# Optimization experiments

Hardware: AMD Instinct MI355X
Metric: run time of the kernel (lower is better)

Reference implementation:

```python
import jax, jax.numpy as jnp
import numpy as np

# --- constants matching DILConfig ---
N_DIFF = 1000      # num_diffusion_steps
STEPS = 4          # inference_steps
S_MAX = 4          # max_scales
BUDGET = 0.2       # entropy_budget
G0 = 2.0           # guidance_strength
ENT_LO = 0.1       # stability_threshold_low
ENT_HI = 0.5       # stability_threshold_high
B, L, C, H = 16, 1024, 128, 512


def setup_inputs() -> dict:
    key = jax.random.key(0)
    ks = jax.random.split(key, 6)
    y_obs = jax.random.normal(ks[0], (B, L, C), dtype=jnp.float32)
    mask = (jax.random.uniform(ks[1], (B, L, C)) > 0.5).astype(jnp.float32)
    z_init = jax.random.normal(ks[2], (B, L, C), dtype=jnp.float32)
    W1 = jax.random.normal(ks[3], (C, H), dtype=jnp.float32) / np.sqrt(C)
    b1 = jnp.zeros((H,), dtype=jnp.float32)
    W2 = jax.random.normal(ks[4], (H, C), dtype=jnp.float32) / np.sqrt(H)
    b2 = jnp.zeros((C,), dtype=jnp.float32)
    tw = jax.random.normal(ks[5], (H,), dtype=jnp.float32)
    return {"y_obs": y_obs, "mask": mask, "z_init": z_init,
            "W1": W1, "b1": b1, "W2": W2, "b2": b2, "tw": tw}


def _dil_forward(y_obs, mask, z_init, W1, b1, W2, b2, tw):
    # diffusion schedule (linear betas)
    betas = jnp.linspace(1e-4, 0.02, N_DIFF, dtype=jnp.float32)
    ac = jnp.cumprod(1.0 - betas)
    alpha = jnp.sqrt(ac)                     # sqrt_alphas_cumprod
    sigma = jnp.sqrt(1.0 - ac)               # sqrt_one_minus_alphas_cumprod
    lam = jnp.log(alpha) - jnp.log(sigma)    # log-SNR/2

    step = N_DIFF // STEPS
    ks = [N_DIFF - 1 - i * step for i in range(STEPS)]

    def score(z, k):
        # epsilon predictor: channel MLP with scalar time feature
        t_feat = jnp.float32(k) / N_DIFF
        h = jax.nn.gelu(jnp.einsum('blc,ch->blh', z, W1) + b1 + t_feat * tw)
        return jnp.einsum('blh,hc->blc', h, W2) + b2

    z = z_init
    for k in ks:  # fixed small unrolled loop over inference steps
        kp = max(k - step, 0)
        eps = score(z, k)                                   # [B,L,C]
        h_lam = lam[kp] - lam[k]
        base_a = alpha[kp] / alpha[k]
        base_b = sigma[kp] * (jnp.exp(h_lam) - 1.0)

        # entropy map: batch-mean |eps| per pixel
        ent_pix = jnp.mean(jnp.abs(eps), axis=0)            # [L,C]

        # self-guidance on observed entries
        obs_err = (z - y_obs) * mask
        guidance = -obs_err / (jnp.var(obs_err) + 1e-8)     # [B,L,C]

        z_new = z
        # coarse -> fine so finer-scale selected nodes overwrite coarser ones
        for s in range(S_MAX - 1, -1, -1):
            w = 2 ** s
            pooled = ent_pix.reshape(L // w, w, C // w, w).mean(axis=(1, 3))
            Knodes = max(1, int(BUDGET * pooled.size))
            _, idx = jax.lax.top_k(pooled.ravel(), Knodes)
            selg = jnp.zeros((pooled.size,), jnp.float32).at[idx].set(1.0)
            selg = selg.reshape(pooled.shape)
            sel = jnp.repeat(jnp.repeat(selg, w, axis=0), w, axis=1)     # [L,C]
            ent_up = jnp.repeat(jnp.repeat(pooled, w, axis=0), w, axis=1)

            # adaptive solver order from entropy stability thresholds
            order = (1.0 + (ent_up > ENT_LO).astype(jnp.float32)
                         + (ent_up > ENT_HI).astype(jnp.float32))
            corr = (1.0 + (order - 1.0) * 0.5 * h_lam
                        + (order - 1.0) * (order - 2.0) / 6.0 * h_lam ** 2)
            gs = G0 * ent_up / (ent_up + 1.0)               # adaptive guidance

            cand = base_a * z - base_b * (corr * eps) + gs * guidance
            z_new = jnp.where(sel[None, :, :] > 0, cand, z_new)
        z = z_new
    return z


def reference(y_obs, mask, z_init, W1, b1, W2, b2, tw):
    return _dil_forward(y_obs, mask, z_init, W1, b1, W2, b2, tw)
```

## Files before the change

### kernel.cpp

```cpp
#include <hip/hip_runtime.h>
#include <math.h>
#include <stdint.h>

#define L_DIM 1024
#define C_DIM 128
#define H_DIM 512
#define B_DIM 16
#define LC (L_DIM * C_DIM)
#define BLC (B_DIM * LC)

typedef __attribute__((ext_vector_type(8))) short short8;
typedef __attribute__((ext_vector_type(4))) float floatx4;

__device__ __forceinline__ unsigned fordbits(unsigned u) {
    return (u & 0x80000000u) ? ~u : (u | 0x80000000u);
}

__device__ __forceinline__ void split3(float x, unsigned& uh, unsigned& um,
                                       unsigned& ul) {
    uh = __float_as_uint(x);
    const float r1 = x - __uint_as_float(uh & 0xffff0000u);
    um = __float_as_uint(r1);
    const float r2 = r1 - __uint_as_float(um & 0xffff0000u);
    ul = __float_as_uint(r2);
}

__device__ __forceinline__ float gelu_fast(float x) {
    const float g = 0.7978845608028654f * (x + 0.044715f * x * x * x);
    const float e = __expf(2.0f * g);
    const float t = 1.0f - 2.0f / (e + 1.0f);
    return 0.5f * x * (1.0f + t);
}

__global__ __launch_bounds__(256) void wsplit_kernel(
    const float* __restrict__ W1, const float* __restrict__ W2,
    unsigned short* __restrict__ W1h, unsigned short* __restrict__ W1m,
    unsigned short* __restrict__ W1l, unsigned short* __restrict__ W2h,
    unsigned short* __restrict__ W2m, unsigned short* __restrict__ W2l) {
    const int t = blockIdx.x * 256 + threadIdx.x;
    unsigned uh, um, ul;
    if (t < 65536) {
        const int j = t & 7, lane = (t >> 3) & 63, nt = (t >> 9) & 31,
                  kt = (t >> 14) & 3;
        const int k = kt * 32 + (lane >> 4) * 8 + j;
        const int n = nt * 16 + (lane & 15);
        split3(W1[k * 512 + n], uh, um, ul);
        W1h[t] = (unsigned short)(uh >> 16);
        W1m[t] = (unsigned short)(um >> 16);
        W1l[t] = (unsigned short)(ul >> 16);
    } else {
        const int t2 = t - 65536;
        const int j = t2 & 7, lane = (t2 >> 3) & 63, nt = (t2 >> 9) & 7,
                  kt = (t2 >> 12) & 15;
        const int k = kt * 32 + (lane >> 4) * 8 + j;
        const int n = nt * 16 + (lane & 15);
        split3(W2[k * 128 + n], uh, um, ul);
        W2h[t2] = (unsigned short)(uh >> 16);
        W2m[t2] = (unsigned short)(um >> 16);
        W2l[t2] = (unsigned short)(ul >> 16);
    }
}

#define MFMA6(AH, AM, AL, BH, BM, BL, ACC)                                    \
    ACC = __builtin_amdgcn_mfma_f32_16x16x32_bf16(AL, BH, ACC, 0, 0, 0);      \
    ACC = __builtin_amdgcn_mfma_f32_16x16x32_bf16(AM, BM, ACC, 0, 0, 0);      \
    ACC = __builtin_amdgcn_mfma_f32_16x16x32_bf16(AH, BL, ACC, 0, 0, 0);      \
    ACC = __builtin_amdgcn_mfma_f32_16x16x32_bf16(AM, BH, ACC, 0, 0, 0);      \
    ACC = __builtin_amdgcn_mfma_f32_16x16x32_bf16(AH, BM, ACC, 0, 0, 0);      \
    ACC = __builtin_amdgcn_mfma_f32_16x16x32_bf16(AH, BH, ACC, 0, 0, 0);

__device__ __forceinline__ int swz(int row, int col) {
    return row * 128 + ((((col >> 3) ^ (row & 15))) << 3) + (col & 7);
}

template <int UPD>
__global__ __launch_bounds__(512, 4) void mlp_kernel(
    float* __restrict__ z, const float* __restrict__ y,
    const float* __restrict__ mk,
    const unsigned short* __restrict__ W1h, const unsigned short* __restrict__ W1m,
    const unsigned short* __restrict__ W1l, const unsigned short* __restrict__ W2h,
    const unsigned short* __restrict__ W2m, const unsigned short* __restrict__ W2l,
    const float* __restrict__ b1, const float* __restrict__ tw,
    const float* __restrict__ b2, float t_feat,
    float* __restrict__ eps_buf, float* __restrict__ ent,
    const float* __restrict__ cA, const float* __restrict__ cB,
    const float* __restrict__ cG, float* __restrict__ accum) {
    __shared__ unsigned short zA[3][4096];
    __shared__ unsigned short hA[3][4096];
    __shared__ float red1[8], red2[8];
    const int tid = threadIdx.x;
    const int w = tid >> 6, lane = tid & 63;
    const int quad = lane >> 4, m16 = lane & 15;
    const int l0 = blockIdx.x * 2;

    float s1 = 0.f, s2 = 0.f;
#pragma unroll
    for (int e = 0; e < 2; ++e) {
        const int f = tid * 8 + e * 4;
        const int r_ = f >> 7, cb = f & 127;
        const int b = r_ & 15, il = r_ >> 4, l = l0 + il;
        const size_t g = ((size_t)b * 1024 + l) * 128 + cb;
        float4 zv = *(const float4*)(z + g);
        const float4 yv = *(const float4*)(y + g);
        const float4 mv = *(const float4*)(mk + g);
        if (UPD) {
            const float4 ev = *(const float4*)(eps_buf + g);
            const int pix = l * 128 + cb;
            const float4 a4 = *(const float4*)(cA + pix);
            const float4 b4 = *(const float4*)(cB + pix);
            const float4 g4 = *(const float4*)(cG + pix);
            zv.x = a4.x * zv.x - b4.x * ev.x - g4.x * ((zv.x - yv.x) * mv.x);
            zv.y = a4.y * zv.y - b4.y * ev.y - g4.y * ((zv.y - yv.y) * mv.y);
            zv.z = a4.z * zv.z - b4.z * ev.z - g4.z * ((zv.z - yv.z) * mv.z);
            zv.w = a4.w * zv.w - b4.w * ev.w - g4.w * ((zv.w - yv.w) * mv.w);
            *(float4*)(z + g) = zv;
        }
        float oe;
        oe = (zv.x - yv.x) * mv.x; s1 += oe; s2 += oe * oe;
        oe = (zv.y - yv.y) * mv.y; s1 += oe; s2 += oe * oe;
        oe = (zv.z - yv.z) * mv.z; s1 += oe; s2 += oe * oe;
        oe = (zv.w - yv.w) * mv.w; s1 += oe; s2 += oe * oe;

        const int base = swz(r_, cb);
        const float xs[4] = {zv.x, zv.y, zv.z, zv.w};
        ushort4 vh, vm, vl;
        unsigned uh, um, ul;
        split3(xs[0], uh, um, ul); vh.x = uh >> 16; vm.x = um >> 16; vl.x = ul >> 16;
        split3(xs[1], uh, um, ul); vh.y = uh >> 16; vm.y = um >> 16; vl.y = ul >> 16;
        split3(xs[2], uh, um, ul); vh.z = uh >> 16; vm.z = um >> 16; vl.z = ul >> 16;
        split3(xs[3], uh, um, ul); vh.w = uh >> 16; vm.w = um >> 16; vl.w = ul >> 16;
        *(ushort4*)(&zA[0][base]) = vh;
        *(ushort4*)(&zA[1][base]) = vm;
        *(ushort4*)(&zA[2][base]) = vl;
    }
#pragma unroll
    for (int off = 32; off; off >>= 1) {
        s1 += __shfl_down(s1, off);
        s2 += __shfl_down(s2, off);
    }
    if (lane == 0) { red1[w] = s1; red2[w] = s2; }
    __syncthreads();
    if (tid == 0) {
        float a1 = 0.f, a2 = 0.f;
#pragma unroll
        for (int i = 0; i < 8; ++i) { a1 += red1[i]; a2 += red2[i]; }
        atomicAdd(&accum[0], a1);
        atomicAdd(&accum[1], a2);
    }

    floatx4 acc1[8];
#pragma unroll
    for (int i = 0; i < 8; ++i) acc1[i] = (floatx4){0.f, 0.f, 0.f, 0.f};

#pragma unroll
    for (int kt = 0; kt < 4; ++kt) {
        short8 Ah[2], Am[2], Al[2];
#pragma unroll
        for (int il = 0; il < 2; ++il) {
            const int fb = swz(il * 16 + m16, kt * 32 + quad * 8);
            Ah[il] = *(const short8*)(&zA[0][fb]);
            Am[il] = *(const short8*)(&zA[1][fb]);
            Al[il] = *(const short8*)(&zA[2][fb]);
        }
#pragma unroll
        for (int q = 0; q < 4; ++q) {
            const size_t off = ((size_t)(kt * 32 + q * 8 + w) * 64 + lane) * 8;
            const short8 bh = *(const short8*)(W1h + off);
            const short8 bm = *(const short8*)(W1m + off);
            const short8 bl = *(const short8*)(W1l + off);
#pragma unroll
            for (int il = 0; il < 2; ++il) {
                floatx4 a = acc1[q * 2 + il];
                MFMA6(Ah[il], Am[il], Al[il], bh, bm, bl, a);
                acc1[q * 2 + il] = a;
            }
        }
    }

    floatx4 acc2[2];
    acc2[0] = (floatx4){0.f, 0.f, 0.f, 0.f};
    acc2[1] = (floatx4){0.f, 0.f, 0.f, 0.f};

    for (int q = 0; q < 4; ++q) {
        __syncthreads();
        {
            const int colg = q * 128 + w * 16 + m16;
            const float bb = b1[colg] + t_feat * tw[colg];
            const int kcol = w * 16 + m16;
#pragma unroll
            for (int il = 0; il < 2; ++il) {
#pragma unroll
                for (int r = 0; r < 4; ++r) {
                    const float x = gelu_fast(acc1[q * 2 + il][r] + bb);
                    unsigned uh, um, ul;
                    split3(x, uh, um, ul);
                    const int idx = swz(il * 16 + quad * 4 + r, kcol);
                    hA[0][idx] = (unsigned short)(uh >> 16);
                    hA[1][idx] = (unsigned short)(um >> 16);
                    hA[2][idx] = (unsigned short)(ul >> 16);
                }
            }
        }
        __syncthreads();

#pragma unroll
        for (int ktl = 0; ktl < 4; ++ktl) {
            short8 Ah2[2], Am2[2], Al2[2];
#pragma unroll
            for (int il = 0; il < 2; ++il) {
                const int fb = swz(il * 16 + m16, ktl * 32 + quad * 8);
                Ah2[il] = *(const short8*)(&hA[0][fb]);
                Am2[il] = *(const short8*)(&hA[1][fb]);
                Al2[il] = *(const short8*)(&hA[2][fb]);
            }
            const size_t off =
                ((size_t)((q * 4 + ktl) * 8 + w) * 64 + lane) * 8;
            const short8 bh = *(const short8*)(W2h + off);
            const short8 bm = *(const short8*)(W2m + off);
            const short8 bl = *(const short8*)(W2l + off);
#pragma unroll
            for (int il = 0; il < 2; ++il) {
                floatx4 a = acc2[il];
                MFMA6(Ah2[il], Am2[il], Al2[il], bh, bm, bl, a);
                acc2[il] = a;
            }
        }
    }

    {
        const int col = w * 16 + m16;
        const float bb2 = b2[col];
#pragma unroll
        for (int il = 0; il < 2; ++il) {
            float pa = 0.f;
#pragma unroll
            for (int r = 0; r < 4; ++r) {
                const float e = acc2[il][r] + bb2;
                const int b = quad * 4 + r;
                eps_buf[((size_t)b * 1024 + l0 + il) * 128 + col] = e;
                pa += fabsf(e);
            }
            pa += __shfl_xor(pa, 16);
            pa += __shfl_xor(pa, 32);
            if (quad == 0) ent[(l0 + il) * 128 + col] = pa * (1.0f / 16.0f);
        }
    }
}


__global__ __launch_bounds__(256) void pools_kernel(
    const float* __restrict__ ent, float* __restrict__ p1,
    float* __restrict__ p2, float* __restrict__ p3,
    unsigned* __restrict__ ghist) {
    __shared__ unsigned lh[16384];
    const int tid = threadIdx.x;
    const int gid = blockIdx.x * 256 + tid;
    for (int i = tid; i < 16384; i += 256) lh[i] = 0u;
    __syncthreads();

    {
        const float2 ev = *(const float2*)(ent + (size_t)gid * 2);
        atomicAdd(&lh[fordbits(__float_as_uint(ev.x)) >> 18], 1u);
        atomicAdd(&lh[fordbits(__float_as_uint(ev.y)) >> 18], 1u);
    }
    if (gid < 32768) {
        const int r = gid >> 6, c = gid & 63;
        float s = 0.f;
#pragma unroll
        for (int ii = 0; ii < 2; ++ii)
#pragma unroll
            for (int jj = 0; jj < 2; ++jj)
                s += ent[((r * 2 + ii) << 7) + c * 2 + jj];
        p1[gid] = s * 0.25f;
    }
    if (gid < 8192) {
        const int r = gid >> 5, c = gid & 31;
        float s = 0.f;
#pragma unroll
        for (int ii = 0; ii < 4; ++ii)
#pragma unroll
            for (int jj = 0; jj < 4; ++jj)
                s += ent[((r * 4 + ii) << 7) + c * 4 + jj];
        p2[gid] = s * 0.0625f;
    }
    if (gid < 2048) {
        const int r = gid >> 4, c = gid & 15;
        float s = 0.f;
#pragma unroll
        for (int ii = 0; ii < 8; ++ii)
#pragma unroll
            for (int jj = 0; jj < 8; ++jj)
                s += ent[((r * 8 + ii) << 7) + c * 8 + jj];
        p3[gid] = s * (1.0f / 64.0f);
    }
    __syncthreads();
    for (int i = tid; i < 16384; i += 256) {
        const unsigned c = lh[i];
        if (c) atomicAdd(&ghist[i], c);
    }
}

#define CAND_CAP 16384

template <int NPT4, int N, unsigned K>
__device__ __forceinline__ void small_select(
    const float* __restrict__ data, unsigned* __restrict__ gout, const int t,
    const int w8, unsigned* __restrict__ histcand,
    unsigned* __restrict__ part, unsigned (*hrep)[512],
    unsigned* sh_b, unsigned* sh_krem, unsigned* sh_cnt, unsigned* sh_d,
    unsigned* sh_k2) {
    float4 xv[NPT4];
#pragma unroll
    for (int i = 0; i < NPT4; ++i) {
        const int idx4 = t + i * 1024;
        if (idx4 < (N >> 2)) xv[i] = ((const float4*)data)[idx4];
        else xv[i] = (float4){-1e30f, -1e30f, -1e30f, -1e30f};
    }
    unsigned u[NPT4 * 4];
#pragma unroll
    for (int i = 0; i < NPT4; ++i) {
        u[4 * i + 0] = fordbits(__float_as_uint(xv[i].x));
        u[4 * i + 1] = fordbits(__float_as_uint(xv[i].y));
        u[4 * i + 2] = fordbits(__float_as_uint(xv[i].z));
        u[4 * i + 3] = fordbits(__float_as_uint(xv[i].w));
    }
    if (t == 0) { *sh_b = 0u; *sh_krem = 1u; *sh_cnt = 0u; *sh_d = 0u; *sh_k2 = 1u; }
    for (int i = t; i < 16384; i += 1024) histcand[i] = 0u;
    __syncthreads();
#pragma unroll
    for (int j = 0; j < NPT4 * 4; ++j) atomicAdd(&histcand[u[j] >> 18], 1u);
    __syncthreads();
    {
        unsigned s = 0;
#pragma unroll
        for (int j = 0; j < 16; ++j) s += histcand[t * 16 + j];
        part[t] = s;
    }
    __syncthreads();
    for (int off = 1; off < 1024; off <<= 1) {
        const unsigned v = (t + off < 1024) ? part[t + off] : 0u;
        __syncthreads();
        part[t] += v;
        __syncthreads();
    }
    {
        const unsigned suf = part[t];
        const unsigned sufn = (t < 1023) ? part[t + 1] : 0u;
        if (suf >= K && sufn < K) {
            unsigned run = sufn;
            for (int b = 15; b >= 0; --b) {
                const unsigned hb = histcand[t * 16 + b];
                run += hb;
                if (run >= K) {
                    *sh_b = (unsigned)(t * 16 + b);
                    *sh_krem = K - (run - hb);
                    break;
                }
            }
        }
    }
    __syncthreads();
    const unsigned b14 = *sh_b;
    unsigned krem = *sh_krem;
    __syncthreads();
#pragma unroll
    for (int j = 0; j < NPT4 * 4; ++j)
        if ((u[j] >> 18) == b14) {
            const unsigned p = atomicAdd(sh_cnt, 1u);
            if (p < CAND_CAP) histcand[p] = u[j];
        }
    __syncthreads();
    const unsigned cnt = *sh_cnt;
    const bool inlds = (cnt <= CAND_CAP);
    for (int i = t; i < 4096; i += 1024) ((unsigned*)hrep)[i] = 0u;
    __syncthreads();
    if (inlds) {
        for (unsigned i = t; i < cnt; i += 1024)
            atomicAdd(&hrep[w8][(histcand[i] >> 9) & 511u], 1u);
    } else {
#pragma unroll
        for (int j = 0; j < NPT4 * 4; ++j)
            if ((u[j] >> 18) == b14)
                atomicAdd(&hrep[w8][(u[j] >> 9) & 511u], 1u);
    }
    __syncthreads();
    if (t < 512) {
        unsigned s = 0;
#pragma unroll
        for (int r = 0; r < 8; ++r) s += hrep[r][t];
        part[t] = s;
    }
    __syncthreads();
    for (int off = 1; off < 512; off <<= 1) {
        unsigned v = 0u;
        if (t < 512) v = (t + off < 512) ? part[t + off] : 0u;
        __syncthreads();
        if (t < 512) part[t] += v;
        __syncthreads();
    }
    if (t < 512) {
        const unsigned suf = part[t];
        const unsigned sufn = (t < 511) ? part[t + 1] : 0u;
        if (suf >= krem && sufn < krem) { *sh_d = (unsigned)t; *sh_k2 = krem - sufn; }
    }
    __syncthreads();
    const unsigned dA = *sh_d;
    krem = *sh_k2;
    __syncthreads();
    for (int i = t; i < 4096; i += 1024) ((unsigned*)hrep)[i] = 0u;
    __syncthreads();
    if (inlds) {
        for (unsigned i = t; i < cnt; i += 1024) {
            const unsigned c = histcand[i];
            if (((c >> 9) & 511u) == dA) atomicAdd(&hrep[w8][c & 511u], 1u);
        }
    } else {
#pragma unroll
        for (int j = 0; j < NPT4 * 4; ++j)
            if ((u[j] >> 18) == b14 && ((u[j] >> 9) & 511u) == dA)
                atomicAdd(&hrep[w8][u[j] & 511u], 1u);
    }
    __syncthreads();
    if (t < 512) {
        unsigned s = 0;
#pragma unroll
        for (int r = 0; r < 8; ++r) s += hrep[r][t];
        part[t] = s;
    }
    __syncthreads();
    for (int off = 1; off < 512; off <<= 1) {
        unsigned v = 0u;
        if (t < 512) v = (t + off < 512) ? part[t + off] : 0u;
        __syncthreads();
        if (t < 512) part[t] += v;
        __syncthreads();
    }
    if (t < 512) {
        const unsigned suf = part[t];
        const unsigned sufn = (t < 511) ? part[t + 1] : 0u;
        if (suf >= krem && sufn < krem)
            gout[0] = (b14 << 18) | (dA << 9) | (unsigned)t;
    }
}

__global__ __launch_bounds__(1024, 1) void thresh_kernel(
    const float* __restrict__ ent, const float* __restrict__ p1,
    const float* __restrict__ p2, const float* __restrict__ p3,
    const unsigned* __restrict__ ghist, unsigned* __restrict__ gprefix) {
    const int scale = blockIdx.x, t = threadIdx.x;
    __shared__ unsigned histcand[16384];
    __shared__ unsigned part[1024];
    __shared__ unsigned hrep[8][512];
    __shared__ unsigned sh_b, sh_krem, sh_cnt, sh_d, sh_k2;
    const int w8 = (t >> 6) & 7;

    if (scale == 1) {
        small_select<8, 32768, 6553u>(p1, &gprefix[1], t, w8, histcand, part,
                                      hrep, &sh_b, &sh_krem, &sh_cnt, &sh_d,
                                      &sh_k2);
        return;
    }
    if (scale == 2) {
        small_select<2, 8192, 1638u>(p2, &gprefix[2], t, w8, histcand, part,
                                     hrep, &sh_b, &sh_krem, &sh_cnt, &sh_d,
                                     &sh_k2);
        return;
    }
    if (scale == 3) {
        small_select<1, 2048, 409u>(p3, &gprefix[3], t, w8, histcand, part,
                                    hrep, &sh_b, &sh_krem, &sh_cnt, &sh_d,
                                    &sh_k2);
        return;
    }

    const unsigned K = 26214u;
    if (t == 0) { sh_b = 0u; sh_krem = 1u; sh_cnt = 0u; sh_d = 0u; sh_k2 = 1u; }

    {
        unsigned s = 0;
        const uint4* h4 = (const uint4*)(ghist + t * 16);
#pragma unroll
        for (int j = 0; j < 4; ++j) {
            const uint4 x = h4[j];
            s += x.x + x.y + x.z + x.w;
        }
        part[t] = s;
    }
    __syncthreads();
    for (int off = 1; off < 1024; off <<= 1) {
        const unsigned v = (t + off < 1024) ? part[t + off] : 0u;
        __syncthreads();
        part[t] += v;
        __syncthreads();
    }
    {
        const unsigned suf = part[t];
        const unsigned sufn = (t < 1023) ? part[t + 1] : 0u;
        if (suf >= K && sufn < K) {
            unsigned run = sufn;
            for (int b = 15; b >= 0; --b) {
                const unsigned hb = ghist[t * 16 + b];
                run += hb;
                if (run >= K) {
                    sh_b = (unsigned)(t * 16 + b);
                    sh_krem = K - (run - hb);
                    break;
                }
            }
        }
    }
    __syncthreads();
    const unsigned b14 = sh_b;
    unsigned krem = sh_krem;

    for (int base = 0; base < 32768; base += 8192) {
        float4 w4[8];
#pragma unroll
        for (int i = 0; i < 8; ++i)
            w4[i] = ((const float4*)ent)[base + i * 1024 + t];
#pragma unroll
        for (int i = 0; i < 8; ++i) {
            const float xs[4] = {w4[i].x, w4[i].y, w4[i].z, w4[i].w};
#pragma unroll
            for (int j = 0; j < 4; ++j) {
                const unsigned uu = fordbits(__float_as_uint(xs[j]));
                if ((uu >> 18) == b14) {
                    const unsigned p = atomicAdd(&sh_cnt, 1u);
                    if (p < CAND_CAP) histcand[p] = uu;
                }
            }
        }
    }
    __syncthreads();
    const unsigned cnt = sh_cnt;
    const bool inlds = (cnt <= CAND_CAP);

    for (int i = t; i < 4096; i += 1024) ((unsigned*)hrep)[i] = 0u;
    __syncthreads();
    if (inlds) {
        for (unsigned i = t; i < cnt; i += 1024)
            atomicAdd(&hrep[w8][(histcand[i] >> 9) & 511u], 1u);
    } else {
        for (int base = 0; base < 32768; base += 8192) {
            float4 w4[8];
#pragma unroll
            for (int i = 0; i < 8; ++i)
                w4[i] = ((const float4*)ent)[base + i * 1024 + t];
#pragma unroll
            for (int i = 0; i < 8; ++i) {
                const float xs[4] = {w4[i].x, w4[i].y, w4[i].z, w4[i].w};
#pragma unroll
                for (int j = 0; j < 4; ++j) {
                    const unsigned uu = fordbits(__float_as_uint(xs[j]));
                    if ((uu >> 18) == b14)
                        atomicAdd(&hrep[w8][(uu >> 9) & 511u], 1u);
                }
            }
        }
    }
    __syncthreads();
    if (t < 512) {
        unsigned s = 0;
#pragma unroll
        for (int r = 0; r < 8; ++r) s += hrep[r][t];
        part[t] = s;
    }
    __syncthreads();
    for (int off = 1; off < 512; off <<= 1) {
        unsigned v = 0u;
        if (t < 512) v = (t + off < 512) ? part[t + off] : 0u;
        __syncthreads();
        if (t < 512) part[t] += v;
        __syncthreads();
    }
    if (t < 512) {
        const unsigned suf = part[t];
        const unsigned sufn = (t < 511) ? part[t + 1] : 0u;
        if (suf >= krem && sufn < krem) { sh_d = (unsigned)t; sh_k2 = krem - sufn; }
    }
    __syncthreads();
    const unsigned dA = sh_d;
    krem = sh_k2;
    __syncthreads();

    for (int i = t; i < 4096; i += 1024) ((unsigned*)hrep)[i] = 0u;
    __syncthreads();
    if (inlds) {
        for (unsigned i = t; i < cnt; i += 1024) {
            const unsigned c = histcand[i];
            if (((c >> 9) & 511u) == dA) atomicAdd(&hrep[w8][c & 511u], 1u);
        }
    } else {
        for (int base = 0; base < 32768; base += 8192) {
            float4 w4[8];
#pragma unroll
            for (int i = 0; i < 8; ++i)
                w4[i] = ((const float4*)ent)[base + i * 1024 + t];
#pragma unroll
            for (int i = 0; i < 8; ++i) {
                const float xs[4] = {w4[i].x, w4[i].y, w4[i].z, w4[i].w};
#pragma unroll
                for (int j = 0; j < 4; ++j) {
                    const unsigned uu = fordbits(__float_as_uint(xs[j]));
                    if ((uu >> 18) == b14 && ((uu >> 9) & 511u) == dA)
                        atomicAdd(&hrep[w8][uu & 511u], 1u);
                }
            }
        }
    }
    __syncthreads();
    if (t < 512) {
        unsigned s = 0;
#pragma unroll
        for (int r = 0; r < 8; ++r) s += hrep[r][t];
        part[t] = s;
    }
    __syncthreads();
    for (int off = 1; off < 512; off <<= 1) {
        unsigned v = 0u;
        if (t < 512) v = (t + off < 512) ? part[t + off] : 0u;
        __syncthreads();
        if (t < 512) part[t] += v;
        __syncthreads();
    }
    if (t < 512) {
        const unsigned suf = part[t];
        const unsigned sufn = (t < 511) ? part[t + 1] : 0u;
        if (suf >= krem && sufn < krem)
            gprefix[0] = (b14 << 18) | (dA << 9) | (unsigned)t;
    }
}

__global__ __launch_bounds__(256) void coeff_kernel(
    const float* __restrict__ ent, const float* __restrict__ p1,
    const float* __restrict__ p2, const float* __restrict__ p3,
    const unsigned* __restrict__ gprefix, const float* __restrict__ accum_si,
    float* __restrict__ cA, float* __restrict__ cB, float* __restrict__ cG,
    unsigned* __restrict__ ghist, float base_a, float base_b, float h_lam) {
    const int i = blockIdx.x * 256 + threadIdx.x;
    if (i < 16384) ghist[i] = 0u;

    const unsigned t0 = gprefix[0], t1 = gprefix[1], t2 = gprefix[2],
                   t3 = gprefix[3];
    const float mean = accum_si[0] * (1.0f / (float)BLC);
    const float var = accum_si[1] * (1.0f / (float)BLC) - mean * mean;
    const float vinv = 1.0f / (var + 1e-8f);

    const int l = i >> 7, c = i & 127;
    float ent_v = 0.f;
    bool sel = false;
    const float v0 = ent[i];
    if (fordbits(__float_as_uint(v0)) >= t0) { ent_v = v0; sel = true; }
    else {
        const float v1 = p1[((l >> 1) << 6) + (c >> 1)];
        if (fordbits(__float_as_uint(v1)) >= t1) { ent_v = v1; sel = true; }
        else {
            const float v2 = p2[((l >> 2) << 5) + (c >> 2)];
            if (fordbits(__float_as_uint(v2)) >= t2) { ent_v = v2; sel = true; }
            else {
                const float v3 = p3[((l >> 3) << 4) + (c >> 3)];
                if (fordbits(__float_as_uint(v3)) >= t3) { ent_v = v3; sel = true; }
            }
        }
    }
    if (sel) {
        float corr;
        if (ent_v > 0.5f)
            corr = 1.0f + h_lam + h_lam * h_lam * (1.0f / 3.0f);
        else if (ent_v > 0.1f)
            corr = 1.0f + 0.5f * h_lam;
        else
            corr = 1.0f;
        cA[i] = base_a;
        cB[i] = base_b * corr;
        cG[i] = (2.0f * ent_v / (ent_v + 1.0f)) * vinv;
    } else {
        cA[i] = 1.0f;
        cB[i] = 0.f;
        cG[i] = 0.f;
    }
}

__global__ __launch_bounds__(256) void update_kernel(
    float* __restrict__ z, const float* __restrict__ y,
    const float* __restrict__ mk, const float* __restrict__ eps,
    const float* __restrict__ cA, const float* __restrict__ cB,
    const float* __restrict__ cG) {
    const int idx = blockIdx.x * 256 + threadIdx.x;
    const int p = idx & (LC - 1);
    const float zi = z[idx];
    z[idx] = cA[p] * zi - cB[p] * eps[idx] - cG[p] * ((zi - y[idx]) * mk[idx]);
}

extern "C" void kernel_launch(void* const* d_in, const int* in_sizes, int n_in,
                              void* d_out, int out_size, void* d_ws,
                              size_t ws_size, hipStream_t stream) {
    const float* y_obs = (const float*)d_in[0];
    const float* mask = (const float*)d_in[1];
    const float* z_init = (const float*)d_in[2];
    const float* W1 = (const float*)d_in[3];
    const float* b1 = (const float*)d_in[4];
    const float* W2 = (const float*)d_in[5];
    const float* b2 = (const float*)d_in[6];
    const float* tw = (const float*)d_in[7];
    float* z = (float*)d_out;
    float* ws = (float*)d_ws;

    float* eps = ws;
    float* ent = ws + 2097152;
    float* p1 = ws + 2228224;
    float* p2 = ws + 2260992;
    float* p3 = ws + 2269184;
    float* cA = ws + 2271232;
    float* cB = ws + 2402304;
    float* cG = ws + 2533376;
    float* accum = ws + 2664448;
    unsigned* gprefix = (unsigned*)(ws + 2664456);
    unsigned* ghist = (unsigned*)(ws + 2664460);
    unsigned short* W1h = (unsigned short*)(ws + 2680844);
    unsigned short* W1m = (unsigned short*)(ws + 2713612);
    unsigned short* W1l = (unsigned short*)(ws + 2746380);
    unsigned short* W2h = (unsigned short*)(ws + 2779148);
    unsigned short* W2m = (unsigned short*)(ws + 2811916);
    unsigned short* W2l = (unsigned short*)(ws + 2844684);

    float alpha_[1000], sigma_[1000], lam_[1000];
    {
        float ac = 1.0f;
        for (int i = 0; i < 1000; ++i) {
            const float beta = 1e-4f + (0.02f - 1e-4f) * ((float)i / 999.0f);
            ac = ac * (1.0f - beta);
            alpha_[i] = sqrtf(ac);
            sigma_[i] = sqrtf(1.0f - ac);
            lam_[i] = logf(alpha_[i]) - logf(sigma_[i]);
        }
    }
    float tf[4], hl[4], ba[4], bb[4];
    for (int si = 0; si < 4; ++si) {
        const int k = 999 - si * 250;
        const int kp = (k - 250 > 0) ? (k - 250) : 0;
        tf[si] = (float)k / 1000.0f;
        hl[si] = lam_[kp] - lam_[k];
        ba[si] = alpha_[kp] / alpha_[k];
        bb[si] = sigma_[kp] * (expf(hl[si]) - 1.0f);
    }

    hipMemcpyAsync(z, z_init, sizeof(float) * BLC, hipMemcpyDeviceToDevice,
                   stream);
    hipMemsetAsync(accum, 0, (8 + 4 + 16384) * sizeof(unsigned), stream);
    wsplit_kernel<<<512, 256, 0, stream>>>(W1, W2, W1h, W1m, W1l, W2h, W2m,
                                           W2l);

    for (int si = 0; si < 4; ++si) {
        if (si == 0) {
            mlp_kernel<0><<<512, 512, 0, stream>>>(
                z, y_obs, mask, W1h, W1m, W1l, W2h, W2m, W2l, b1, tw, b2,
                tf[0], eps, ent, cA, cB, cG, accum);
        } else {
            mlp_kernel<1><<<512, 512, 0, stream>>>(
                z, y_obs, mask, W1h, W1m, W1l, W2h, W2m, W2l, b1, tw, b2,
                tf[si], eps, ent, cA, cB, cG, accum + 2 * si);
        }
        pools_kernel<<<256, 256, 0, stream>>>(ent, p1, p2, p3, ghist);
        thresh_kernel<<<4, 1024, 0, stream>>>(ent, p1, p2, p3, ghist, gprefix);
        coeff_kernel<<<512, 256, 0, stream>>>(ent, p1, p2, p3, gprefix,
                                              accum + 2 * si, cA, cB, cG,
                                              ghist, ba[si], bb[si], hl[si]);
    }
    update_kernel<<<8192, 256, 0, stream>>>(z, y_obs, mask, eps, cA, cB, cG);
}
```

Baseline: 388.6 us.

## Remove memcpy/memset, fuse final update into coeff, double-buffer hidden LDS

The initial z copy and the accumulator memset are dropped: the first MLP steps read z_init directly and the weight-split kernel zeroes the accumulators. The final update kernel is folded into a templated coeff kernel that applies the per-pixel coefficients across the batch. The MLP's second GEMM now alternates between two LDS buffers for hidden activations, and one per-chunk __syncthreads is removed. The pooling histogram packs two 16-bit counts per shared word and uses vector loads. The lost barrier and the 16-bit counters carry race and overflow risk.

```diff
diff --git a/kernel.cpp b/kernel.cpp
--- a/kernel.cpp
+++ b/kernel.cpp
@@ -36,8 +36,10 @@
     const float* __restrict__ W1, const float* __restrict__ W2,
     unsigned short* __restrict__ W1h, unsigned short* __restrict__ W1m,
     unsigned short* __restrict__ W1l, unsigned short* __restrict__ W2h,
-    unsigned short* __restrict__ W2m, unsigned short* __restrict__ W2l) {
+    unsigned short* __restrict__ W2m, unsigned short* __restrict__ W2l,
+    unsigned* __restrict__ zeroblk) {
     const int t = blockIdx.x * 256 + threadIdx.x;
+    if (t < 16396) zeroblk[t] = 0u;
     unsigned uh, um, ul;
     if (t < 65536) {
         const int j = t & 7, lane = (t >> 3) & 63, nt = (t >> 9) & 31,
@@ -75,8 +77,8 @@
 
 template <int UPD>
 __global__ __launch_bounds__(512, 4) void mlp_kernel(
-    float* __restrict__ z, const float* __restrict__ y,
-    const float* __restrict__ mk,
+    float* __restrict__ z, const float* __restrict__ zr,
+    const float* __restrict__ y, const float* __restrict__ mk,
     const unsigned short* __restrict__ W1h, const unsigned short* __restrict__ W1m,
     const unsigned short* __restrict__ W1l, const unsigned short* __restrict__ W2h,
     const unsigned short* __restrict__ W2m, const unsigned short* __restrict__ W2l,
@@ -85,8 +87,7 @@
     float* __restrict__ eps_buf, float* __restrict__ ent,
     const float* __restrict__ cA, const float* __restrict__ cB,
     const float* __restrict__ cG, float* __restrict__ accum) {
-    __shared__ unsigned short zA[3][4096];
-    __shared__ unsigned short hA[3][4096];
+    __shared__ unsigned short lds2[2][3][4096];
     __shared__ float red1[8], red2[8];
     const int tid = threadIdx.x;
     const int w = tid >> 6, lane = tid & 63;
@@ -100,7 +101,7 @@
         const int r_ = f >> 7, cb = f & 127;
         const int b = r_ & 15, il = r_ >> 4, l = l0 + il;
         const size_t g = ((size_t)b * 1024 + l) * 128 + cb;
-        float4 zv = *(const float4*)(z + g);
+        float4 zv = *(const float4*)(zr + g);
         const float4 yv = *(const float4*)(y + g);
         const float4 mv = *(const float4*)(mk + g);
         if (UPD) {
@@ -129,9 +130,9 @@
         split3(xs[1], uh, um, ul); vh.y = uh >> 16; vm.y = um >> 16; vl.y = ul >> 16;
         split3(xs[2], uh, um, ul); vh.z = uh >> 16; vm.z = um >> 16; vl.z = ul >> 16;
         split3(xs[3], uh, um, ul); vh.w = uh >> 16; vm.w = um >> 16; vl.w = ul >> 16;
-        *(ushort4*)(&zA[0][base]) = vh;
-        *(ushort4*)(&zA[1][base]) = vm;
-        *(ushort4*)(&zA[2][base]) = vl;
+        *(ushort4*)(&lds2[0][0][base]) = vh;
+        *(ushort4*)(&lds2[0][1][base]) = vm;
+        *(ushort4*)(&lds2[0][2][base]) = vl;
     }
 #pragma unroll
     for (int off = 32; off; off >>= 1) {
@@ -158,9 +159,9 @@
 #pragma unroll
         for (int il = 0; il < 2; ++il) {
             const int fb = swz(il * 16 + m16, kt * 32 + quad * 8);
-            Ah[il] = *(const short8*)(&zA[0][fb]);
-            Am[il] = *(const short8*)(&zA[1][fb]);
-            Al[il] = *(const short8*)(&zA[2][fb]);
+            Ah[il] = *(const short8*)(&lds2[0][0][fb]);
+            Am[il] = *(const short8*)(&lds2[0][1][fb]);
+            Al[il] = *(const short8*)(&lds2[0][2][fb]);
         }
 #pragma unroll
         for (int q = 0; q < 4; ++q) {
@@ -181,8 +182,9 @@
     acc2[0] = (floatx4){0.f, 0.f, 0.f, 0.f};
     acc2[1] = (floatx4){0.f, 0.f, 0.f, 0.f};
 
+#pragma unroll
     for (int q = 0; q < 4; ++q) {
-        __syncthreads();
+        const int bi = (q & 1) ^ 1;
         {
             const int colg = q * 128 + w * 16 + m16;
             const float bb = b1[colg] + t_feat * tw[colg];
@@ -195,9 +197,9 @@
                     unsigned uh, um, ul;
                     split3(x, uh, um, ul);
                     const int idx = swz(il * 16 + quad * 4 + r, kcol);
-                    hA[0][idx] = (unsigned short)(uh >> 16);
-                    hA[1][idx] = (unsigned short)(um >> 16);
-                    hA[2][idx] = (unsigned short)(ul >> 16);
+                    lds2[bi][0][idx] = (unsigned short)(uh >> 16);
+                    lds2[bi][1][idx] = (unsigned short)(um >> 16);
+                    lds2[bi][2][idx] = (unsigned short)(ul >> 16);
                 }
             }
         }
@@ -209,9 +211,9 @@
 #pragma unroll
             for (int il = 0; il < 2; ++il) {
                 const int fb = swz(il * 16 + m16, ktl * 32 + quad * 8);
-                Ah2[il] = *(const short8*)(&hA[0][fb]);
-                Am2[il] = *(const short8*)(&hA[1][fb]);
-                Al2[il] = *(const short8*)(&hA[2][fb]);
+                Ah2[il] = *(const short8*)(&lds2[bi][0][fb]);
+                Am2[il] = *(const short8*)(&lds2[bi][1][fb]);
+                Al2[il] = *(const short8*)(&lds2[bi][2][fb]);
             }
             const size_t off =
                 ((size_t)((q * 4 + ktl) * 8 + w) * 64 + lane) * 8;
@@ -252,51 +254,56 @@
     const float* __restrict__ ent, float* __restrict__ p1,
     float* __restrict__ p2, float* __restrict__ p3,
     unsigned* __restrict__ ghist) {
-    __shared__ unsigned lh[16384];
+    __shared__ unsigned lh[8192];
     const int tid = threadIdx.x;
     const int gid = blockIdx.x * 256 + tid;
-    for (int i = tid; i < 16384; i += 256) lh[i] = 0u;
+    for (int i = tid; i < 8192; i += 256) lh[i] = 0u;
     __syncthreads();
 
     {
         const float2 ev = *(const float2*)(ent + (size_t)gid * 2);
-        atomicAdd(&lh[fordbits(__float_as_uint(ev.x)) >> 18], 1u);
-        atomicAdd(&lh[fordbits(__float_as_uint(ev.y)) >> 18], 1u);
+        const unsigned b0 = fordbits(__float_as_uint(ev.x)) >> 18;
+        const unsigned b1_ = fordbits(__float_as_uint(ev.y)) >> 18;
+        atomicAdd(&lh[b0 >> 1], 1u << ((b0 & 1) << 4));
+        atomicAdd(&lh[b1_ >> 1], 1u << ((b1_ & 1) << 4));
     }
     if (gid < 32768) {
         const int r = gid >> 6, c = gid & 63;
         float s = 0.f;
 #pragma unroll
-        for (int ii = 0; ii < 2; ++ii)
-#pragma unroll
-            for (int jj = 0; jj < 2; ++jj)
-                s += ent[((r * 2 + ii) << 7) + c * 2 + jj];
+        for (int ii = 0; ii < 2; ++ii) {
+            const float2 e = *(const float2*)(ent + (((r * 2 + ii) << 7) + c * 2));
+            s += e.x; s += e.y;
+        }
         p1[gid] = s * 0.25f;
     }
     if (gid < 8192) {
         const int r = gid >> 5, c = gid & 31;
         float s = 0.f;
 #pragma unroll
-        for (int ii = 0; ii < 4; ++ii)
-#pragma unroll
-            for (int jj = 0; jj < 4; ++jj)
-                s += ent[((r * 4 + ii) << 7) + c * 4 + jj];
+        for (int ii = 0; ii < 4; ++ii) {
+            const float4 e = *(const float4*)(ent + (((r * 4 + ii) << 7) + c * 4));
+            s += e.x; s += e.y; s += e.z; s += e.w;
+        }
         p2[gid] = s * 0.0625f;
     }
     if (gid < 2048) {
         const int r = gid >> 4, c = gid & 15;
         float s = 0.f;
 #pragma unroll
-        for (int ii = 0; ii < 8; ++ii)
-#pragma unroll
-            for (int jj = 0; jj < 8; ++jj)
-                s += ent[((r * 8 + ii) << 7) + c * 8 + jj];
+        for (int ii = 0; ii < 8; ++ii) {
+            const float4 ea = *(const float4*)(ent + (((r * 8 + ii) << 7) + c * 8));
+            const float4 eb = *(const float4*)(ent + (((r * 8 + ii) << 7) + c * 8 + 4));
+            s += ea.x; s += ea.y; s += ea.z; s += ea.w;
+            s += eb.x; s += eb.y; s += eb.z; s += eb.w;
+        }
         p3[gid] = s * (1.0f / 64.0f);
     }
     __syncthreads();
-    for (int i = tid; i < 16384; i += 256) {
-        const unsigned c = lh[i];
-        if (c) atomicAdd(&ghist[i], c);
+    for (int i = tid; i < 8192; i += 256) {
+        const unsigned v = lh[i];
+        if (v & 0xFFFFu) atomicAdd(&ghist[2 * i], v & 0xFFFFu);
+        if (v >> 16) atomicAdd(&ghist[2 * i + 1], v >> 16);
     }
 }
 
@@ -631,14 +638,17 @@
     }
 }
 
+template <int FINAL>
 __global__ __launch_bounds__(256) void coeff_kernel(
     const float* __restrict__ ent, const float* __restrict__ p1,
     const float* __restrict__ p2, const float* __restrict__ p3,
     const unsigned* __restrict__ gprefix, const float* __restrict__ accum_si,
     float* __restrict__ cA, float* __restrict__ cB, float* __restrict__ cG,
-    unsigned* __restrict__ ghist, float base_a, float base_b, float h_lam) {
+    unsigned* __restrict__ ghist, float* __restrict__ z,
+    const float* __restrict__ y, const float* __restrict__ mk,
+    const float* __restrict__ eps, float base_a, float base_b, float h_lam) {
     const int i = blockIdx.x * 256 + threadIdx.x;
-    if (i < 16384) ghist[i] = 0u;
+    if (!FINAL && i < 16384) ghist[i] = 0u;
 
     const unsigned t0 = gprefix[0], t1 = gprefix[1], t2 = gprefix[2],
                    t3 = gprefix[3];
@@ -663,6 +673,7 @@
             }
         }
     }
+    float ca, cb, cg;
     if (sel) {
         float corr;
         if (ent_v > 0.5f)
@@ -671,25 +682,22 @@
             corr = 1.0f + 0.5f * h_lam;
         else
             corr = 1.0f;
-        cA[i] = base_a;
-        cB[i] = base_b * corr;
-        cG[i] = (2.0f * ent_v / (ent_v + 1.0f)) * vinv;
+        ca = base_a;
+        cb = base_b * corr;
+        cg = (2.0f * ent_v / (ent_v + 1.0f)) * vinv;
     } else {
-        cA[i] = 1.0f;
-        cB[i] = 0.f;
-        cG[i] = 0.f;
-    }
-}
-
-__global__ __launch_bounds__(256) void update_kernel(
-    float* __restrict__ z, const float* __restrict__ y,
-    const float* __restrict__ mk, const float* __restrict__ eps,
-    const float* __restrict__ cA, const float* __restrict__ cB,
-    const float* __restrict__ cG) {
-    const int idx = blockIdx.x * 256 + threadIdx.x;
-    const int p = idx & (LC - 1);
-    const float zi = z[idx];
-    z[idx] = cA[p] * zi - cB[p] * eps[idx] - cG[p] * ((zi - y[idx]) * mk[idx]);
+        ca = 1.0f; cb = 0.f; cg = 0.f;
+    }
+    if (!FINAL) {
+        cA[i] = ca; cB[i] = cb; cG[i] = cg;
+    } else {
+#pragma unroll
+        for (int b = 0; b < 16; ++b) {
+            const size_t g = (size_t)b * LC + i;
+            const float zi = z[g];
+            z[g] = ca * zi - cb * eps[g] - cg * ((zi - y[g]) * mk[g]);
+        }
+    }
 }
 
 extern "C" void kernel_launch(void* const* d_in, const int* in_sizes, int n_in,
@@ -745,27 +753,30 @@
         bb[si] = sigma_[kp] * (expf(hl[si]) - 1.0f);
     }
 
-    hipMemcpyAsync(z, z_init, sizeof(float) * BLC, hipMemcpyDeviceToDevice,
-                   stream);
-    hipMemsetAsync(accum, 0, (8 + 4 + 16384) * sizeof(unsigned), stream);
     wsplit_kernel<<<512, 256, 0, stream>>>(W1, W2, W1h, W1m, W1l, W2h, W2m,
-                                           W2l);
+                                           W2l, (unsigned*)accum);
 
     for (int si = 0; si < 4; ++si) {
+        const float* zrd = (si <= 1) ? z_init : z;
         if (si == 0) {
             mlp_kernel<0><<<512, 512, 0, stream>>>(
-                z, y_obs, mask, W1h, W1m, W1l, W2h, W2m, W2l, b1, tw, b2,
+                z, zrd, y_obs, mask, W1h, W1m, W1l, W2h, W2m, W2l, b1, tw, b2,
                 tf[0], eps, ent, cA, cB, cG, accum);
         } else {
             mlp_kernel<1><<<512, 512, 0, stream>>>(
-                z, y_obs, mask, W1h, W1m, W1l, W2h, W2m, W2l, b1, tw, b2,
+                z, zrd, y_obs, mask, W1h, W1m, W1l, W2h, W2m, W2l, b1, tw, b2,
                 tf[si], eps, ent, cA, cB, cG, accum + 2 * si);
         }
         pools_kernel<<<256, 256, 0, stream>>>(ent, p1, p2, p3, ghist);
         thresh_kernel<<<4, 1024, 0, stream>>>(ent, p1, p2, p3, ghist, gprefix);
-        coeff_kernel<<<512, 256, 0, stream>>>(ent, p1, p2, p3, gprefix,
-                                              accum + 2 * si, cA, cB, cG,
-                                              ghist, ba[si], bb[si], hl[si]);
-    }
-    update_kernel<<<8192, 256, 0, stream>>>(z, y_obs, mask, eps, cA, cB, cG);
-}
+        if (si < 3) {
+            coeff_kernel<0><<<512, 256, 0, stream>>>(
+                ent, p1, p2, p3, gprefix, accum + 2 * si, cA, cB, cG, ghist,
+                z, y_obs, mask, eps, ba[si], bb[si], hl[si]);
+        } else {
+            coeff_kernel<1><<<512, 256, 0, stream>>>(
+                ent, p1, p2, p3, gprefix, accum + 2 * si, cA, cB, cG, ghist,
+                z, y_obs, mask, eps, ba[si], bb[si], hl[si]);
+        }
+    }
+}
```

New measurement: 400.2 us. 1.03x slower.
